# Performance work log

Hardware: AMD Instinct MI355X
Metric: run time of the kernel (lower is better)

The kernel has to match this reference:

```python
import jax, jax.numpy as jnp
import numpy as np

BATCH, SEQ, D_MODEL = 2, 2048, 1024
D_STATE, D_CONV = 16, 4
DT_RANK = 64  # ceil(d_model / 16)


def setup_inputs() -> dict:
    key = jax.random.key(0)
    ks = jax.random.split(key, 9)
    x = jax.random.normal(ks[0], (BATCH, SEQ, D_MODEL), jnp.float32)
    conv_w = jax.random.normal(ks[1], (D_MODEL, 1, D_CONV), jnp.float32) * 0.3
    conv_b = jax.random.normal(ks[2], (D_MODEL,), jnp.float32) * 0.1
    x_proj_dt_w = jax.random.normal(ks[3], (DT_RANK, D_MODEL), jnp.float32) * (D_MODEL ** -0.5)
    s = DT_RANK ** -0.5
    dt_proj_w = jax.random.uniform(ks[4], (D_MODEL, DT_RANK), jnp.float32, -s, s)
    dt = jnp.exp(jax.random.uniform(ks[5], (D_MODEL,), jnp.float32)
                 * (np.log(0.1) - np.log(0.001)) + np.log(0.001))
    dt_proj_b = dt + jnp.log(-jnp.expm1(-dt))  # inverse-softplus init
    B_proj_w = jax.random.normal(ks[6], (D_STATE, D_MODEL), jnp.float32) * (D_MODEL ** -0.5)
    C_proj_w = jax.random.normal(ks[7], (D_STATE, D_MODEL), jnp.float32) * (D_MODEL ** -0.5)
    A_log = jnp.log(jnp.tile(jnp.arange(1, D_STATE + 1, dtype=jnp.float32), (D_MODEL, 1)))
    D_param = jnp.ones((D_MODEL,), jnp.float32)
    return dict(x=x, conv_w=conv_w, conv_b=conv_b, x_proj_dt_w=x_proj_dt_w,
                dt_proj_w=dt_proj_w, dt_proj_b=dt_proj_b, B_proj_w=B_proj_w,
                C_proj_w=C_proj_w, A_log=A_log, D_param=D_param)


def _forward(x, conv_w, conv_b, x_proj_dt_w, dt_proj_w, dt_proj_b,
             B_proj_w, C_proj_w, A_log, D_param):
    B, L, D = x.shape
    # causal depthwise conv1d (torch pads k-1 both sides then trims to L == left-pad k-1)
    xc = jax.lax.conv_general_dilated(
        x.transpose(0, 2, 1), conv_w, window_strides=(1,),
        padding=[(D_CONV - 1, 0)], feature_group_count=D,
        dimension_numbers=('NCH', 'OIH', 'NCH'))  # (B, D, L)
    xc = jax.nn.silu((xc + conv_b[None, :, None]).transpose(0, 2, 1))  # (B, L, D)

    dt = jax.nn.softplus((xc @ x_proj_dt_w.T) @ dt_proj_w.T + dt_proj_b)  # (B, L, D)
    B_ssm = xc @ B_proj_w.T  # (B, L, N)
    C_ssm = xc @ C_proj_w.T  # (B, L, N)

    A = -jnp.exp(A_log)                                    # (D, N)
    dA = jnp.exp(dt[..., None] * A)                        # (B, L, D, N)
    dBx = dt[..., None] * B_ssm[:, :, None, :] * xc[..., None]  # (B, L, D, N)

    def step(h, inp):
        dA_t, dBx_t, C_t = inp
        h = dA_t * h + dBx_t                               # (B, D, N)
        y_t = jnp.einsum('bdn,bn->bd', h, C_t)
        return h, y_t

    h0 = jnp.zeros((B, D, D_STATE), x.dtype)
    _, ys = jax.lax.scan(step, h0,
                         (dA.transpose(1, 0, 2, 3),
                          dBx.transpose(1, 0, 2, 3),
                          C_ssm.transpose(1, 0, 2)))
    return ys.transpose(1, 0, 2) + D_param * xc  # (B, L, D)


def reference(x, conv_w, conv_b, x_proj_dt_w, dt_proj_w, dt_proj_b,
              B_proj_w, C_proj_w, A_log, D_param):
    return _forward(x, conv_w, conv_b, x_proj_dt_w, dt_proj_w, dt_proj_b,
                    B_proj_w, C_proj_w, A_log, D_param)
```

## Files before the change

kernel.cpp:

```cpp
#include <hip/hip_runtime.h>
#include <math.h>

#define BATCH 2
#define SEQ   2048
#define DM    1024
#define NS    16
#define RK    64
#define NCH   128
#define CL    (SEQ / NCH)
#define NPROJ 96

#define LOG2E 1.4426950408889634f

typedef __attribute__((ext_vector_type(8))) short bf16x8;
typedef __attribute__((ext_vector_type(4))) float f32x4;

#if __has_builtin(__builtin_amdgcn_exp2f)
__device__ __forceinline__ float fexp2(float x) { return __builtin_amdgcn_exp2f(x); }
#else
__device__ __forceinline__ float fexp2(float x) { return exp2f(x); }
#endif

__device__ __forceinline__ unsigned short f2bf(float f) {
    union { float f; unsigned int u; } v; v.f = f;
    unsigned int u = v.u;
    u += 0x7FFFu + ((u >> 16) & 1u);
    return (unsigned short)(u >> 16);
}

__global__ __launch_bounds__(256) void k_conv(const float* __restrict__ x,
    const float* __restrict__ cw, const float* __restrict__ cb,
    float* __restrict__ xc, unsigned short* __restrict__ xcb)
{
    int idx = blockIdx.x * 256 + threadIdx.x;
    int d = idx & (DM - 1);
    int l = (idx >> 10) & (SEQ - 1);
    float4 w = *(const float4*)(cw + d * 4);
    float acc = cb[d];
    float x0 = (l >= 3) ? x[idx - 3 * DM] : 0.f;
    float x1 = (l >= 2) ? x[idx - 2 * DM] : 0.f;
    float x2 = (l >= 1) ? x[idx - 1 * DM] : 0.f;
    float x3 = x[idx];
    acc = fmaf(x0, w.x, acc);
    acc = fmaf(x1, w.y, acc);
    acc = fmaf(x2, w.z, acc);
    acc = fmaf(x3, w.w, acc);
    float e = __expf(-acc);
    float s = acc / (1.f + e);
    xc[idx] = s;
    xcb[idx] = f2bf(s);
}

__global__ __launch_bounds__(256) void k_twdt(const float* __restrict__ w,
                                              float* __restrict__ wt)
{
    int t = blockIdx.x * 256 + threadIdx.x;
    int d = t & (DM - 1);
    int r = t >> 10;
    wt[t] = w[d * RK + r];
}

__global__ __launch_bounds__(256) void k_wprep(const float* __restrict__ wx,
    const float* __restrict__ wb, const float* __restrict__ wc,
    unsigned short* __restrict__ wf)
{
    int idx = blockIdx.x * 256 + threadIdx.x;
    int i    = idx & 7;
    int lane = (idx >> 3) & 63;
    int s    = (idx >> 9) & 31;
    int t    = idx >> 14;
    int j = t * 16 + (lane & 15);
    int k = s * 32 + ((lane >> 4) << 3) + i;
    float v = (j < 64) ? wx[(size_t)j * DM + k]
            : (j < 80) ? wb[(size_t)(j - 64) * DM + k]
                       : wc[(size_t)(j - 80) * DM + k];
    wf[idx] = f2bf(v);
}

__global__ __launch_bounds__(64) void k_proj(const unsigned short* __restrict__ xcb,
    const unsigned short* __restrict__ wf, float* __restrict__ dl,
    float* __restrict__ Bs, float* __restrict__ Cs)
{
    int lane = threadIdx.x;
    int r0 = blockIdx.x * 16;
    int m = lane & 15, q = lane >> 4;
    f32x4 acc[6];
    #pragma unroll
    for (int t = 0; t < 6; t++) acc[t] = (f32x4){0.f, 0.f, 0.f, 0.f};

    const unsigned short* ap = xcb + (size_t)(r0 + m) * DM + q * 8;
    #pragma unroll 4
    for (int s = 0; s < 32; s++) {
        bf16x8 a = *(const bf16x8*)(ap + s * 32);
        #pragma unroll
        for (int t = 0; t < 6; t++) {
            bf16x8 b = *(const bf16x8*)(wf + (size_t)((t * 32 + s) * 64 + lane) * 8);
            acc[t] = __builtin_amdgcn_mfma_f32_16x16x32_bf16(a, b, acc[t], 0, 0, 0);
        }
    }
    #pragma unroll
    for (int t = 0; t < 6; t++) {
        #pragma unroll
        for (int i = 0; i < 4; i++) {
            int row = r0 + q * 4 + i;
            int col = t * 16 + m;
            float v = acc[t][i];
            if (col < 64)      dl[(size_t)row * RK + col] = v;
            else if (col < 80) Bs[(size_t)row * NS + (col - 64)] = v;
            else               Cs[(size_t)row * NS + (col - 80)] = v;
        }
    }
}

__global__ __launch_bounds__(256) void k_dt(const float* __restrict__ dl,
    const float* __restrict__ wt, const float* __restrict__ bias,
    float* __restrict__ dt)
{
    __shared__ __align__(16) float lr[16][RK];
    int tid = threadIdx.x;
    int row0 = blockIdx.x * 16;
    ((float4*)&lr[0][0])[tid] = ((const float4*)(dl + (size_t)row0 * RK))[tid];
    __syncthreads();
    int d0 = tid * 4;
    float4 acc[16];
    #pragma unroll
    for (int mm = 0; mm < 16; mm++) acc[mm] = make_float4(0.f, 0.f, 0.f, 0.f);
    for (int r = 0; r < RK; r++) {
        float4 w = *(const float4*)(wt + (size_t)r * DM + d0);
        #pragma unroll
        for (int mm = 0; mm < 16; mm++) {
            float lv = lr[mm][r];
            acc[mm].x = fmaf(lv, w.x, acc[mm].x);
            acc[mm].y = fmaf(lv, w.y, acc[mm].y);
            acc[mm].z = fmaf(lv, w.z, acc[mm].z);
            acc[mm].w = fmaf(lv, w.w, acc[mm].w);
        }
    }
    float4 b = *(const float4*)(bias + d0);
    #pragma unroll
    for (int mm = 0; mm < 16; mm++) {
        float4 z = make_float4(acc[mm].x + b.x, acc[mm].y + b.y,
                               acc[mm].z + b.z, acc[mm].w + b.w);
        float4 o;
        o.x = fmaxf(z.x, 0.f) + __logf(1.f + __expf(-fabsf(z.x)));
        o.y = fmaxf(z.y, 0.f) + __logf(1.f + __expf(-fabsf(z.y)));
        o.z = fmaxf(z.z, 0.f) + __logf(1.f + __expf(-fabsf(z.z)));
        o.w = fmaxf(z.w, 0.f) + __logf(1.f + __expf(-fabsf(z.w)));
        *(float4*)(dt + (size_t)(row0 + mm) * DM + d0) = o;
    }
}

__global__ __launch_bounds__(256) void k_scan1(const float* __restrict__ dt,
    const float* __restrict__ xc, const float* __restrict__ Bs,
    const float* __restrict__ alog, float* __restrict__ S,
    float* __restrict__ sdtA)
{
    int d = blockIdx.x * 256 + threadIdx.x;
    int c = blockIdx.y;
    int b = blockIdx.z;
    float a2[NS], h[NS];
    #pragma unroll
    for (int n = 0; n < NS; n++) {
        a2[n] = -__expf(alog[d * NS + n]) * LOG2E;
        h[n] = 0.f;
    }
    int l0 = c * CL;
    const float* dtp = dt + ((size_t)(b * SEQ + l0)) * DM + d;
    const float* xcp = xc + ((size_t)(b * SEQ + l0)) * DM + d;
    const float* bp  = Bs + ((size_t)(b * SEQ + l0)) * NS;
    float sdt = 0.f;
    #pragma unroll 4
    for (int i = 0; i < CL; i++) {
        float dtv = dtp[(size_t)i * DM];
        float xcv = xcp[(size_t)i * DM];
        float dbx = dtv * xcv;
        sdt += dtv;
        #pragma unroll
        for (int n = 0; n < NS; n++) {
            float e = fexp2(dtv * a2[n]);
            h[n] = fmaf(e, h[n], dbx * bp[i * NS + n]);
        }
    }
    float* sp = S + (((size_t)(b * NCH + c) * DM) + d) * NS;
    #pragma unroll
    for (int n = 0; n < NS; n += 4)
        *(float4*)(sp + n) = make_float4(h[n], h[n + 1], h[n + 2], h[n + 3]);
    sdtA[(size_t)(b * NCH + c) * DM + d] = sdt;
}

__global__ __launch_bounds__(256) void k_scan2(float* __restrict__ S,
    const float* __restrict__ sdtA, const float* __restrict__ alog)
{
    int t = blockIdx.x * 256 + threadIdx.x;
    int n = t & (NS - 1);
    int d = (t >> 4) & (DM - 1);
    int b = t >> 14;
    float a2 = -__expf(alog[d * NS + n]) * LOG2E;
    float H = 0.f;
    for (int c = 0; c < NCH; c++) {
        size_t idx = (((size_t)(b * NCH + c) * DM) + d) * NS + n;
        float Sv = S[idx];
        float sd = sdtA[(size_t)(b * NCH + c) * DM + d];
        S[idx] = H;
        H = fmaf(fexp2(a2 * sd), H, Sv);
    }
}

__global__ __launch_bounds__(256) void k_scan3(const float* __restrict__ dt,
    const float* __restrict__ xc, const float* __restrict__ Bs,
    const float* __restrict__ Cs, const float* __restrict__ alog,
    const float* __restrict__ Dp, const float* __restrict__ S,
    float* __restrict__ out)
{
    int d = blockIdx.x * 256 + threadIdx.x;
    int c = blockIdx.y;
    int b = blockIdx.z;
    float a2[NS], h[NS];
    const float* hp = S + (((size_t)(b * NCH + c) * DM) + d) * NS;
    #pragma unroll
    for (int n = 0; n < NS; n++) {
        a2[n] = -__expf(alog[d * NS + n]) * LOG2E;
        h[n] = hp[n];
    }
    float dpv = Dp[d];
    int l0 = c * CL;
    const float* dtp = dt + ((size_t)(b * SEQ + l0)) * DM + d;
    const float* xcp = xc + ((size_t)(b * SEQ + l0)) * DM + d;
    const float* bp  = Bs + ((size_t)(b * SEQ + l0)) * NS;
    const float* cp  = Cs + ((size_t)(b * SEQ + l0)) * NS;
    float* op = out + ((size_t)(b * SEQ + l0)) * DM + d;
    #pragma unroll 2
    for (int i = 0; i < CL; i++) {
        float dtv = dtp[(size_t)i * DM];
        float xcv = xcp[(size_t)i * DM];
        float dbx = dtv * xcv;
        float y = 0.f;
        #pragma unroll
        for (int n = 0; n < NS; n++) {
            float e = fexp2(dtv * a2[n]);
            h[n] = fmaf(e, h[n], dbx * bp[i * NS + n]);
            y = fmaf(h[n], cp[i * NS + n], y);
        }
        op[(size_t)i * DM] = fmaf(dpv, xcv, y);
    }
}

extern "C" void kernel_launch(void* const* d_in, const int* in_sizes, int n_in,
                              void* d_out, int out_size, void* d_ws, size_t ws_size,
                              hipStream_t stream)
{
    const float* x    = (const float*)d_in[0];
    const float* cw   = (const float*)d_in[1];
    const float* cb   = (const float*)d_in[2];
    const float* wxp  = (const float*)d_in[3];
    const float* wdt  = (const float*)d_in[4];
    const float* bdt  = (const float*)d_in[5];
    const float* wb   = (const float*)d_in[6];
    const float* wc   = (const float*)d_in[7];
    const float* alog = (const float*)d_in[8];
    const float* dpar = (const float*)d_in[9];
    float* out = (float*)d_out;
    float* ws  = (float*)d_ws;

    float* xc = ws;
    float* dt = ws + 4194304;
    float* dl = ws + 8388608;
    float* Bs = ws + 8650752;
    float* Cs = ws + 8716288;
    float* S  = ws + 8781824;
    float* sd = ws + 12976128;
    float* wt = ws + 13238272;
    unsigned short* wf = (unsigned short*)(ws + 13303808);
    unsigned short* xcb = (unsigned short*)S;

    k_conv <<<dim3(BATCH * SEQ * DM / 256), dim3(256), 0, stream>>>(x, cw, cb, xc, xcb);
    k_twdt <<<dim3(RK * DM / 256),          dim3(256), 0, stream>>>(wdt, wt);
    k_wprep<<<dim3(NPROJ * DM / 256),       dim3(256), 0, stream>>>(wxp, wb, wc, wf);
    k_proj <<<dim3(BATCH * SEQ / 16),       dim3(64),  0, stream>>>(xcb, wf, dl, Bs, Cs);
    k_dt   <<<dim3(BATCH * SEQ / 16),       dim3(256), 0, stream>>>(dl, wt, bdt, dt);
    k_scan1<<<dim3(DM / 256, NCH, BATCH),   dim3(256), 0, stream>>>(dt, xc, Bs, alog, S, sd);
    k_scan2<<<dim3(BATCH * DM * NS / 256),  dim3(256), 0, stream>>>(S, sd, alog);
    k_scan3<<<dim3(DM / 256, NCH, BATCH),   dim3(256), 0, stream>>>(dt, xc, Bs, Cs, alog, dpar, S, out);
}
```

Before: 166.7 us.

## Split inter-chunk scan into two-level hierarchy, drop fp32 xc copy, merge prep kernels

The serial 128-step inter-chunk state scan becomes a two-level scan. Groups of 16 chunks are scanned in parallel, a short 8-step pass combines the group ends, and scan3 applies the group start state decayed by the cumulative dt. The fp32 copy of the conv output is dropped so the scans read the bf16 copy, which cuts write and read traffic but lowers the precision of the skip term and dBx. The two weight-prep kernels are merged into one launch, and one extra launch is added for the hierarchical scan.

```diff
diff --git a/kernel.cpp b/kernel.cpp
--- a/kernel.cpp
+++ b/kernel.cpp
@@ -8,6 +8,8 @@
 #define RK    64
 #define NCH   128
 #define CL    (SEQ / NCH)
+#define NGRP  8
+#define GC    16
 #define NPROJ 96
 
 #define LOG2E 1.4426950408889634f
@@ -27,10 +29,14 @@
     u += 0x7FFFu + ((u >> 16) & 1u);
     return (unsigned short)(u >> 16);
 }
+__device__ __forceinline__ float bf2f(unsigned short s) {
+    union { unsigned int u; float f; } v; v.u = ((unsigned int)s) << 16;
+    return v.f;
+}
 
 __global__ __launch_bounds__(256) void k_conv(const float* __restrict__ x,
     const float* __restrict__ cw, const float* __restrict__ cb,
-    float* __restrict__ xc, unsigned short* __restrict__ xcb)
+    unsigned short* __restrict__ xcb)
 {
     int idx = blockIdx.x * 256 + threadIdx.x;
     int d = idx & (DM - 1);
@@ -47,34 +53,32 @@
     acc = fmaf(x3, w.w, acc);
     float e = __expf(-acc);
     float s = acc / (1.f + e);
-    xc[idx] = s;
     xcb[idx] = f2bf(s);
 }
 
-__global__ __launch_bounds__(256) void k_twdt(const float* __restrict__ w,
-                                              float* __restrict__ wt)
-{
-    int t = blockIdx.x * 256 + threadIdx.x;
-    int d = t & (DM - 1);
-    int r = t >> 10;
-    wt[t] = w[d * RK + r];
-}
-
-__global__ __launch_bounds__(256) void k_wprep(const float* __restrict__ wx,
+__global__ __launch_bounds__(256) void k_prep(const float* __restrict__ w,
+    float* __restrict__ wt, const float* __restrict__ wx,
     const float* __restrict__ wb, const float* __restrict__ wc,
     unsigned short* __restrict__ wf)
 {
-    int idx = blockIdx.x * 256 + threadIdx.x;
-    int i    = idx & 7;
-    int lane = (idx >> 3) & 63;
-    int s    = (idx >> 9) & 31;
-    int t    = idx >> 14;
-    int j = t * 16 + (lane & 15);
-    int k = s * 32 + ((lane >> 4) << 3) + i;
-    float v = (j < 64) ? wx[(size_t)j * DM + k]
-            : (j < 80) ? wb[(size_t)(j - 64) * DM + k]
-                       : wc[(size_t)(j - 80) * DM + k];
-    wf[idx] = f2bf(v);
+    int t = blockIdx.x * 256 + threadIdx.x;
+    if (t < RK * DM) {
+        int d = t & (DM - 1);
+        int r = t >> 10;
+        wt[t] = w[d * RK + r];
+    } else {
+        int idx = t - RK * DM;
+        int i    = idx & 7;
+        int lane = (idx >> 3) & 63;
+        int s    = (idx >> 9) & 31;
+        int tt   = idx >> 14;
+        int j = tt * 16 + (lane & 15);
+        int k = s * 32 + ((lane >> 4) << 3) + i;
+        float v = (j < 64) ? wx[(size_t)j * DM + k]
+                : (j < 80) ? wb[(size_t)(j - 64) * DM + k]
+                           : wc[(size_t)(j - 80) * DM + k];
+        wf[idx] = f2bf(v);
+    }
 }
 
 __global__ __launch_bounds__(64) void k_proj(const unsigned short* __restrict__ xcb,
@@ -151,7 +155,7 @@
 }
 
 __global__ __launch_bounds__(256) void k_scan1(const float* __restrict__ dt,
-    const float* __restrict__ xc, const float* __restrict__ Bs,
+    const unsigned short* __restrict__ xcb, const float* __restrict__ Bs,
     const float* __restrict__ alog, float* __restrict__ S,
     float* __restrict__ sdtA)
 {
@@ -166,13 +170,13 @@
     }
     int l0 = c * CL;
     const float* dtp = dt + ((size_t)(b * SEQ + l0)) * DM + d;
-    const float* xcp = xc + ((size_t)(b * SEQ + l0)) * DM + d;
+    const unsigned short* xcp = xcb + ((size_t)(b * SEQ + l0)) * DM + d;
     const float* bp  = Bs + ((size_t)(b * SEQ + l0)) * NS;
     float sdt = 0.f;
     #pragma unroll 4
     for (int i = 0; i < CL; i++) {
         float dtv = dtp[(size_t)i * DM];
-        float xcv = xcp[(size_t)i * DM];
+        float xcv = bf2f(xcp[(size_t)i * DM]);
         float dbx = dtv * xcv;
         sdt += dtv;
         #pragma unroll
@@ -188,8 +192,38 @@
     sdtA[(size_t)(b * NCH + c) * DM + d] = sdt;
 }
 
-__global__ __launch_bounds__(256) void k_scan2(float* __restrict__ S,
-    const float* __restrict__ sdtA, const float* __restrict__ alog)
+__global__ __launch_bounds__(256) void k_s2a(float* __restrict__ S,
+    const float* __restrict__ sd, float* __restrict__ csd,
+    float* __restrict__ Gend, float* __restrict__ Gsd,
+    const float* __restrict__ alog)
+{
+    int t = blockIdx.x * 256 + threadIdx.x;
+    int n = t & (NS - 1);
+    int d = (t >> 4) & (DM - 1);
+    int g = (t >> 14) & (NGRP - 1);
+    int b = t >> 17;
+    float a2 = -__expf(alog[d * NS + n]) * LOG2E;
+    float H = 0.f, cum = 0.f;
+    int c0 = g * GC;
+    #pragma unroll
+    for (int i = 0; i < GC; i++) {
+        int c = c0 + i;
+        size_t sidx = (((size_t)(b * NCH + c) * DM) + d) * NS + n;
+        size_t didx = (size_t)(b * NCH + c) * DM + d;
+        float Sv = S[sidx];
+        float sdv = sd[didx];
+        S[sidx] = H;
+        H = fmaf(fexp2(a2 * sdv), H, Sv);
+        if (n == 0) csd[didx] = cum;
+        cum += sdv;
+    }
+    Gend[t] = H;
+    if (n == 0) Gsd[(size_t)(b * NGRP + g) * DM + d] = cum;
+}
+
+__global__ __launch_bounds__(256) void k_s2b(const float* __restrict__ Gend,
+    const float* __restrict__ Gsd, const float* __restrict__ alog,
+    float* __restrict__ Gstart)
 {
     int t = blockIdx.x * 256 + threadIdx.x;
     int n = t & (NS - 1);
@@ -197,42 +231,47 @@
     int b = t >> 14;
     float a2 = -__expf(alog[d * NS + n]) * LOG2E;
     float H = 0.f;
-    for (int c = 0; c < NCH; c++) {
-        size_t idx = (((size_t)(b * NCH + c) * DM) + d) * NS + n;
-        float Sv = S[idx];
-        float sd = sdtA[(size_t)(b * NCH + c) * DM + d];
-        S[idx] = H;
-        H = fmaf(fexp2(a2 * sd), H, Sv);
+    #pragma unroll
+    for (int g = 0; g < NGRP; g++) {
+        size_t gi = (((size_t)(b * NGRP + g) * DM) + d) * NS + n;
+        float Gv = Gend[gi];
+        float sdv = Gsd[(size_t)(b * NGRP + g) * DM + d];
+        Gstart[gi] = H;
+        H = fmaf(fexp2(a2 * sdv), H, Gv);
     }
 }
 
 __global__ __launch_bounds__(256) void k_scan3(const float* __restrict__ dt,
-    const float* __restrict__ xc, const float* __restrict__ Bs,
+    const unsigned short* __restrict__ xcb, const float* __restrict__ Bs,
     const float* __restrict__ Cs, const float* __restrict__ alog,
     const float* __restrict__ Dp, const float* __restrict__ S,
+    const float* __restrict__ csd, const float* __restrict__ Gstart,
     float* __restrict__ out)
 {
     int d = blockIdx.x * 256 + threadIdx.x;
     int c = blockIdx.y;
     int b = blockIdx.z;
+    int g = c >> 4;
     float a2[NS], h[NS];
-    const float* hp = S + (((size_t)(b * NCH + c) * DM) + d) * NS;
+    const float* sp = S + (((size_t)(b * NCH + c) * DM) + d) * NS;
+    const float* gp = Gstart + (((size_t)(b * NGRP + g) * DM) + d) * NS;
+    float cum = csd[(size_t)(b * NCH + c) * DM + d];
     #pragma unroll
     for (int n = 0; n < NS; n++) {
         a2[n] = -__expf(alog[d * NS + n]) * LOG2E;
-        h[n] = hp[n];
+        h[n] = fmaf(fexp2(a2[n] * cum), gp[n], sp[n]);
     }
     float dpv = Dp[d];
     int l0 = c * CL;
     const float* dtp = dt + ((size_t)(b * SEQ + l0)) * DM + d;
-    const float* xcp = xc + ((size_t)(b * SEQ + l0)) * DM + d;
+    const unsigned short* xcp = xcb + ((size_t)(b * SEQ + l0)) * DM + d;
     const float* bp  = Bs + ((size_t)(b * SEQ + l0)) * NS;
     const float* cp  = Cs + ((size_t)(b * SEQ + l0)) * NS;
     float* op = out + ((size_t)(b * SEQ + l0)) * DM + d;
     #pragma unroll 2
     for (int i = 0; i < CL; i++) {
         float dtv = dtp[(size_t)i * DM];
-        float xcv = xcp[(size_t)i * DM];
+        float xcv = bf2f(xcp[(size_t)i * DM]);
         float dbx = dtv * xcv;
         float y = 0.f;
         #pragma unroll
@@ -262,23 +301,26 @@
     float* out = (float*)d_out;
     float* ws  = (float*)d_ws;
 
-    float* xc = ws;
-    float* dt = ws + 4194304;
-    float* dl = ws + 8388608;
-    float* Bs = ws + 8650752;
-    float* Cs = ws + 8716288;
-    float* S  = ws + 8781824;
-    float* sd = ws + 12976128;
-    float* wt = ws + 13238272;
-    unsigned short* wf = (unsigned short*)(ws + 13303808);
-    unsigned short* xcb = (unsigned short*)S;
-
-    k_conv <<<dim3(BATCH * SEQ * DM / 256), dim3(256), 0, stream>>>(x, cw, cb, xc, xcb);
-    k_twdt <<<dim3(RK * DM / 256),          dim3(256), 0, stream>>>(wdt, wt);
-    k_wprep<<<dim3(NPROJ * DM / 256),       dim3(256), 0, stream>>>(wxp, wb, wc, wf);
-    k_proj <<<dim3(BATCH * SEQ / 16),       dim3(64),  0, stream>>>(xcb, wf, dl, Bs, Cs);
-    k_dt   <<<dim3(BATCH * SEQ / 16),       dim3(256), 0, stream>>>(dl, wt, bdt, dt);
-    k_scan1<<<dim3(DM / 256, NCH, BATCH),   dim3(256), 0, stream>>>(dt, xc, Bs, alog, S, sd);
-    k_scan2<<<dim3(BATCH * DM * NS / 256),  dim3(256), 0, stream>>>(S, sd, alog);
-    k_scan3<<<dim3(DM / 256, NCH, BATCH),   dim3(256), 0, stream>>>(dt, xc, Bs, Cs, alog, dpar, S, out);
-}
+    float* dt   = ws;
+    float* dl   = ws + 4194304;
+    float* Bs   = ws + 4456448;
+    float* Cs   = ws + 4521984;
+    float* S    = ws + 4587520;
+    float* sd   = ws + 8781824;
+    float* csd  = ws + 9043968;
+    float* wt   = ws + 9306112;
+    float* Gend = ws + 9371648;
+    float* Gst  = ws + 9633792;
+    float* Gsd  = ws + 9895936;
+    unsigned short* wf  = (unsigned short*)(ws + 9912320);
+    unsigned short* xcb = (unsigned short*)(ws + 9961472);
+
+    k_conv <<<dim3(BATCH * SEQ * DM / 256),        dim3(256), 0, stream>>>(x, cw, cb, xcb);
+    k_prep <<<dim3((RK * DM + NPROJ * DM) / 256),  dim3(256), 0, stream>>>(wdt, wt, wxp, wb, wc, wf);
+    k_proj <<<dim3(BATCH * SEQ / 16),              dim3(64),  0, stream>>>(xcb, wf, dl, Bs, Cs);
+    k_dt   <<<dim3(BATCH * SEQ / 16),              dim3(256), 0, stream>>>(dl, wt, bdt, dt);
+    k_scan1<<<dim3(DM / 256, NCH, BATCH),          dim3(256), 0, stream>>>(dt, xcb, Bs, alog, S, sd);
+    k_s2a  <<<dim3(BATCH * NGRP * DM * NS / 256),  dim3(256), 0, stream>>>(S, sd, csd, Gend, Gsd, alog);
+    k_s2b  <<<dim3(BATCH * DM * NS / 256),         dim3(256), 0, stream>>>(Gend, Gsd, alog, Gst);
+    k_scan3<<<dim3(DM / 256, NCH, BATCH),          dim3(256), 0, stream>>>(dt, xcb, Bs, Cs, alog, dpar, S, csd, Gst, out);
+}
```

After: 163.4 us. -2.0%, faster.
